# Performance work log

Hardware: AMD Instinct MI355X
Metric: run time of the kernel (lower is better)

Reference implementation:

```python
import jax, jax.numpy as jnp
import numpy as np

B, S, DM = 4, 2048, 512
H, D = 8, 64          # att_head, head_dim = att_dim // att_head
LEFT, RIGHT = 128, 128  # band_part(left_mask, right_mask)
LARGE = 1e30          # masked_softmax large number for fp32


def setup_inputs() -> dict:
    key = jax.random.key(0)
    ks = jax.random.split(key, 11)
    scale = 1.0 / np.sqrt(DM)
    x = jax.random.normal(ks[0], (B, S, DM), jnp.float32)
    Wq = jax.random.normal(ks[1], (DM, DM), jnp.float32) * scale
    bq = jnp.zeros((DM,), jnp.float32)
    Wk = jax.random.normal(ks[2], (DM, DM), jnp.float32) * scale
    bk = jnp.zeros((DM,), jnp.float32)
    Wv = jax.random.normal(ks[3], (DM, DM), jnp.float32) * scale
    bv = jnp.zeros((DM,), jnp.float32)
    Wo = jax.random.normal(ks[4], (DM, DM), jnp.float32) * scale
    bo = jnp.zeros((DM,), jnp.float32)
    x_len = jax.random.randint(ks[5], (B,), 0, 2048)
    return {"x": x, "Wq": Wq, "bq": bq, "Wk": Wk, "bk": bk,
            "Wv": Wv, "bv": bv, "Wo": Wo, "bo": bo, "x_len": x_len}


def reference(x, Wq, bq, Wk, bk, Wv, bv, Wo, bo, x_len):
    b, s, _ = x.shape
    # QKV projections, split into heads: [B,S,H,D]
    q = (x @ Wq + bq).reshape(b, s, H, D)
    k = (x @ Wk + bk).reshape(b, s, H, D)
    v = (x @ Wv + bv).reshape(b, s, H, D)
    # content energy: [B,H,Q,K], scaled by sqrt(head_dim)
    energy = jnp.einsum('bind,bjnd->bnij', q, k) / jnp.sqrt(jnp.float32(D))
    # banded mask (tf.linalg.band_part semantics): keep -LEFT <= j-i <= RIGHT
    i = jnp.arange(s)[:, None]
    j = jnp.arange(s)[None, :]
    band = ((j - i) <= RIGHT) & ((i - j) <= LEFT)            # [S,S]
    # key-length mask (tf.sequence_mask, expanded to [B,1,1,S])
    seq = jnp.arange(s)[None, :] < x_len[:, None]            # [B,S]
    mask = (band[None, None, :, :] & seq[:, None, None, :]).astype(energy.dtype)
    # masked softmax: energy - (1 - mask) * LARGE, softmax over keys
    att = jax.nn.softmax(energy - (1.0 - mask) * LARGE, axis=-1)
    # context: [B,Q,H,D] -> [B,S,H*D]
    ctx = jnp.einsum('bnij,bjnd->bind', att, v).reshape(b, s, H * D)
    # output projection (use_proj=True)
    return ctx @ Wo + bo
```

## Files before the change

### kernel.cpp

```cpp
#include <hip/hip_runtime.h>

#define S_LEN 2048
#define BATCH 4
#define DMODEL 512
#define NHEAD 8
#define HDIM 64
#define ROWS (BATCH * S_LEN)

using short8 = __attribute__((ext_vector_type(8))) short;
using f32x4  = __attribute__((ext_vector_type(4))) float;

__device__ __forceinline__ unsigned short f2bf(float f) {
  unsigned int u = __builtin_bit_cast(unsigned int, f);
  u += 0x7fffu + ((u >> 16) & 1u);
  return (unsigned short)(u >> 16);
}
__device__ __forceinline__ float bf2f(unsigned short h) {
  unsigned int u = ((unsigned int)h) << 16;
  return __builtin_bit_cast(float, u);
}
__device__ __forceinline__ void glds16(const void* g, void* l) {
  __builtin_amdgcn_global_load_lds((const __attribute__((address_space(1))) unsigned*)g,
                                   (__attribute__((address_space(3))) unsigned*)l, 16, 0, 0);
}

__global__ __launch_bounds__(256) void prep_kernel(const float* __restrict__ x,
                                                   const float* __restrict__ Wq,
                                                   const float* __restrict__ Wk,
                                                   const float* __restrict__ Wv,
                                                   const float* __restrict__ Wo,
                                                   unsigned short* __restrict__ xb,
                                                   unsigned short* __restrict__ WqkT,
                                                   unsigned short* __restrict__ WvT,
                                                   unsigned short* __restrict__ WoT,
                                                   float* __restrict__ xpart) {
  __shared__ float t[32][33];
  const int blk = blockIdx.x, tid = threadIdx.x;
  if (blk < 2048) {
    const int base = (blk * 256 + tid) * 8;
    float4 f0 = *(const float4*)(x + base);
    float4 f1 = *(const float4*)(x + base + 4);
    uint4 o;
    o.x = (unsigned)f2bf(f0.x) | ((unsigned)f2bf(f0.y) << 16);
    o.y = (unsigned)f2bf(f0.z) | ((unsigned)f2bf(f0.w) << 16);
    o.z = (unsigned)f2bf(f1.x) | ((unsigned)f2bf(f1.y) << 16);
    o.w = (unsigned)f2bf(f1.z) | ((unsigned)f2bf(f1.w) << 16);
    *(uint4*)(xb + base) = o;
    return;
  }
  if (blk < 3072) {
    const int tb = blk - 2048;
    const int which = tb >> 8, tile = tb & 255;
    const float* W = which == 0 ? Wq : which == 1 ? Wk : which == 2 ? Wv : Wo;
    unsigned short* WT = which == 0 ? WqkT : which == 1 ? (WqkT + 512 * 512)
                        : which == 2 ? WvT : WoT;
    const int tx = tid & 31, ty = tid >> 5;
    const int x0 = (tile & 15) * 32, y0 = (tile >> 4) * 32;
#pragma unroll
    for (int r = 0; r < 4; r++)
      t[ty + 8 * r][tx] = W[(size_t)(y0 + ty + 8 * r) * DMODEL + x0 + tx];
    __syncthreads();
#pragma unroll
    for (int r = 0; r < 4; r++)
      WT[(size_t)(x0 + ty + 8 * r) * DMODEL + y0 + tx] = f2bf(t[tx][ty + 8 * r]);
    return;
  }
  const int u = blk - 3072;
  const int b = u >> 4, cg = (u >> 3) & 1, rc = u & 7;
  const float* base = x + (size_t)(b * S_LEN + rc * 256) * DMODEL + cg * 256 + tid;
  float s = 0.f;
  for (int j = 0; j < 256; j++) s += base[(size_t)j * DMODEL];
  xpart[u * 256 + tid] = s;
}

__global__ __launch_bounds__(256, 2) void qkv_kernel(const unsigned short* __restrict__ xb,
                                                     const unsigned short* __restrict__ WqkT,
                                                     const unsigned short* __restrict__ WvT,
                                                     const float* __restrict__ bq,
                                                     const float* __restrict__ bk,
                                                     const float* __restrict__ bv,
                                                     const int* __restrict__ x_len,
                                                     const float* __restrict__ xpart,
                                                     unsigned short* __restrict__ Qb,
                                                     unsigned short* __restrict__ Kb,
                                                     unsigned short* __restrict__ Vt,
                                                     float* __restrict__ vsum) {
  __shared__ __align__(16) char smem[16384];
  const int bid = blockIdx.x;
  const int tid = threadIdx.x;
  if (bid >= 768) {
    const int u = bid - 768;
    const int b = u >> 5;
    const int wave = tid >> 6, lane = tid & 63;
    const int cg = lane >> 5, ko = (lane & 31) * 8;
    float xs[8] = {};
#pragma unroll
    for (int rc = 0; rc < 8; rc++) {
      const float* p = xpart + ((b * 16 + cg * 8 + rc) << 8) + ko;
      float4 a0 = *(const float4*)p;
      float4 a1 = *(const float4*)(p + 4);
      xs[0] += a0.x; xs[1] += a0.y; xs[2] += a0.z; xs[3] += a0.w;
      xs[4] += a1.x; xs[5] += a1.y; xs[6] += a1.z; xs[7] += a1.w;
    }
#pragma unroll
    for (int ci = 0; ci < 4; ci++) {
      const int f = (u & 31) * 16 + wave * 4 + ci;
      const uint4 wv = *(const uint4*)(WvT + (size_t)f * DMODEL + lane * 8);
      const unsigned int w[4] = {wv.x, wv.y, wv.z, wv.w};
      float acc = 0.f;
#pragma unroll
      for (int e = 0; e < 4; e++) {
        acc += xs[2 * e] * bf2f((unsigned short)(w[e] & 0xffffu));
        acc += xs[2 * e + 1] * bf2f((unsigned short)(w[e] >> 16));
      }
#pragma unroll
      for (int off = 1; off < 64; off <<= 1) acc += __shfl_xor(acc, off, 64);
      if (lane == 0) vsum[b * DMODEL + f] = acc + 2048.f * bv[f];
    }
    return;
  }
  const bool vmode = bid < 256;
  const unsigned short *A, *Bt;
  int m0, n0;
  if (vmode) {
    m0 = (bid & 3) * 128;
    n0 = (bid >> 2) * 128;
    A = WvT; Bt = xb;
  } else {
    const int q = bid - 256;
    m0 = (q >> 3) * 128;
    n0 = (q & 7) * 128;
    A = xb; Bt = WqkT;
    const int xl = x_len[m0 >> 11];
    const int s0 = m0 & 2047;
    if (n0 >= DMODEL) { if (s0 >= xl) return; }
    else if (s0 >= xl + 128) return;
  }
  char* As = smem;
  char* Bs = smem + 8192;
  const int wave = tid >> 6, lane = tid & 63;
  const int wr = wave >> 1, wc = wave & 1;
  const int lm = lane & 15, lq = lane >> 4;
  const int lr = lane >> 2;
  const int lc = (lane & 3) ^ ((lane >> 3) & 3);
  const unsigned short* gA0 = A + (size_t)(m0 + wave * 16 + lr) * DMODEL + lc * 8;
  const unsigned short* gA1 = A + (size_t)(m0 + (wave + 4) * 16 + lr) * DMODEL + lc * 8;
  const unsigned short* gB0 = Bt + (size_t)(n0 + wave * 16 + lr) * DMODEL + lc * 8;
  const unsigned short* gB1 = Bt + (size_t)(n0 + (wave + 4) * 16 + lr) * DMODEL + lc * 8;
  char* lA0 = As + wave * 1024 + lane * 16;
  char* lA1 = As + (wave + 4) * 1024 + lane * 16;
  char* lB0 = Bs + wave * 1024 + lane * 16;
  char* lB1 = Bs + (wave + 4) * 1024 + lane * 16;
  const int sw = (lm >> 1) & 3;
  int aoff[4], boff[4];
#pragma unroll
  for (int mi = 0; mi < 4; mi++) aoff[mi] = (wr * 64 + mi * 16 + lm) * 64 + (lq ^ sw) * 16;
#pragma unroll
  for (int ni = 0; ni < 4; ni++) boff[ni] = (wc * 64 + ni * 16 + lm) * 64 + (lq ^ sw) * 16;
  f32x4 acc[4][4] = {};
  for (int k0 = 0; k0 < DMODEL; k0 += 32) {
    __syncthreads();
    glds16(gA0 + k0, lA0);
    glds16(gA1 + k0, lA1);
    glds16(gB0 + k0, lB0);
    glds16(gB1 + k0, lB1);
    __syncthreads();
    short8 af[4], bfr[4];
#pragma unroll
    for (int mi = 0; mi < 4; mi++) af[mi] = *(const short8*)(As + aoff[mi]);
#pragma unroll
    for (int ni = 0; ni < 4; ni++) bfr[ni] = *(const short8*)(Bs + boff[ni]);
#pragma unroll
    for (int mi = 0; mi < 4; mi++)
#pragma unroll
      for (int ni = 0; ni < 4; ni++)
        acc[mi][ni] = __builtin_amdgcn_mfma_f32_16x16x32_bf16(af[mi], bfr[ni], acc[mi][ni], 0, 0, 0);
  }
#pragma unroll
  for (int mi = 0; mi < 4; mi++) {
    const int row0 = m0 + wr * 64 + mi * 16 + lq * 4;
#pragma unroll
    for (int ni = 0; ni < 4; ni++) {
      const int col = n0 + wc * 64 + ni * 16 + lm;
#pragma unroll
      for (int r = 0; r < 4; r++) {
        const int row = row0 + r;
        const float v = acc[mi][ni][r];
        if (vmode) {
          Vt[(size_t)row * ROWS + col] = f2bf(v + bv[row]);
        } else if (col < DMODEL) {
          Qb[(size_t)row * DMODEL + col] = f2bf(v + bq[col]);
        } else {
          Kb[(size_t)row * DMODEL + (col - DMODEL)] = f2bf(v + bk[col - DMODEL]);
        }
      }
    }
  }
}

__global__ __launch_bounds__(256) void attn_kernel(const unsigned short* __restrict__ Q,
                                                   const unsigned short* __restrict__ K,
                                                   const unsigned short* __restrict__ Vt,
                                                   const int* __restrict__ x_len,
                                                   const float* __restrict__ vsum,
                                                   const unsigned short* __restrict__ WoT,
                                                   const float* __restrict__ bo,
                                                   float* __restrict__ trow,
                                                   unsigned short* __restrict__ ctx) {
  __shared__ unsigned short Ks[32][72];
  __shared__ unsigned short Vs[64][40];
  __shared__ unsigned short Ps[4][16][40];
  const int tid = threadIdx.x;
  const int unit = blockIdx.x;
  const int wave = tid >> 6, lane = tid & 63;
  if (unit >= 1024) {
    const int u = unit - 1024;
    const int b = u >> 4;
    const float* vs = vsum + b * DMODEL + lane * 8;
    float vreg[8];
    *(float4*)vreg = *(const float4*)vs;
    *(float4*)(vreg + 4) = *(const float4*)(vs + 4);
#pragma unroll
    for (int ci = 0; ci < 8; ci++) {
      const int c = (u & 15) * 32 + wave * 8 + ci;
      const uint4 wv = *(const uint4*)(WoT + (size_t)c * DMODEL + lane * 8);
      const unsigned int w[4] = {wv.x, wv.y, wv.z, wv.w};
      float acc = 0.f;
#pragma unroll
      for (int e = 0; e < 4; e++) {
        acc += vreg[2 * e] * bf2f((unsigned short)(w[e] & 0xffffu));
        acc += vreg[2 * e + 1] * bf2f((unsigned short)(w[e] >> 16));
      }
#pragma unroll
      for (int off = 1; off < 64; off <<= 1) acc += __shfl_xor(acc, off, 64);
      if (lane == 0) trow[b * DMODEL + c] = bo[c] + acc * (1.f / 2048.f);
    }
    return;
  }
  const int b = unit >> 8, h = (unit >> 5) & 7;
  const int i0 = (unit & 31) * 64;
  const int xlen = x_len[b];
  const int t0 = min(S_LEN, xlen + 128);
  if ((i0 & ~127) >= t0) return;
  const int lm = lane & 15, lq = lane >> 4;
  const int q0 = i0 + wave * 16;
  const size_t qoff = (size_t)(b * S_LEN + q0 + lm) * DMODEL + h * HDIM + lq * 8;
  const short8 aq0 = *(const short8*)(Q + qoff);
  const short8 aq1 = *(const short8*)(Q + qoff + 32);
  const int krow = tid >> 3, kchk = (tid & 7) * 8;
  const int vdim = tid >> 2, vchk = (tid & 3) * 8;
  f32x4 oacc[4] = {};
  float lrow[4] = {0.f, 0.f, 0.f, 0.f};
  for (int kt = 0; kt < 10; kt++) {
    const int jt0 = i0 - 128 + kt * 32;
    if (jt0 + 31 < 0 || jt0 >= xlen) continue;
    __syncthreads();
    {
      const int jr = jt0 + krow;
      const int jrc = min(max(jr, 0), S_LEN - 1);
      *(uint4*)&Ks[krow][kchk] =
          *(const uint4*)(K + (size_t)(b * S_LEN + jrc) * DMODEL + h * HDIM + kchk);
      const int jv = jt0 + vchk;
      const int jvc = min(max(jv, 0), S_LEN - 8);
      *(uint4*)&Vs[vdim][vchk] =
          *(const uint4*)(Vt + (size_t)(h * HDIM + vdim) * ROWS + b * S_LEN + jvc);
    }
    __syncthreads();
    if (jt0 + 31 < q0 - 128 || jt0 > q0 + 143) continue;
    f32x4 sv[2];
#pragma unroll
    for (int sub = 0; sub < 2; sub++) {
      const short8 bk0 = *(const short8*)&Ks[sub * 16 + lm][lq * 8];
      const short8 bk1 = *(const short8*)&Ks[sub * 16 + lm][32 + lq * 8];
      f32x4 s = {};
      s = __builtin_amdgcn_mfma_f32_16x16x32_bf16(aq0, bk0, s, 0, 0, 0);
      s = __builtin_amdgcn_mfma_f32_16x16x32_bf16(aq1, bk1, s, 0, 0, 0);
      sv[sub] = s;
    }
    float p[2][4];
#pragma unroll
    for (int sub = 0; sub < 2; sub++) {
      const int j = jt0 + sub * 16 + lm;
      const bool jv = (j >= 0) && (j < xlen);
#pragma unroll
      for (int r = 0; r < 4; r++) {
        const int i = q0 + lq * 4 + r;
        const bool ok = jv && (j - i <= 128) && (i - j <= 128);
        const float pv = ok ? __expf(sv[sub][r] * 0.125f) : 0.f;
        p[sub][r] = pv;
        lrow[r] += pv;
      }
    }
#pragma unroll
    for (int r = 0; r < 4; r++) {
      Ps[wave][lq * 4 + r][lm] = f2bf(p[0][r]);
      Ps[wave][lq * 4 + r][16 + lm] = f2bf(p[1][r]);
    }
    const short8 pf = *(const short8*)&Ps[wave][lm][lq * 8];
#pragma unroll
    for (int dt = 0; dt < 4; dt++) {
      const short8 bv = *(const short8*)&Vs[dt * 16 + lm][lq * 8];
      oacc[dt] = __builtin_amdgcn_mfma_f32_16x16x32_bf16(pf, bv, oacc[dt], 0, 0, 0);
    }
  }
#pragma unroll
  for (int r = 0; r < 4; r++)
#pragma unroll
    for (int off = 1; off < 16; off <<= 1) lrow[r] += __shfl_xor(lrow[r], off, 64);
#pragma unroll
  for (int r = 0; r < 4; r++) {
    const int i = q0 + lq * 4 + r;
    const size_t obase = (size_t)(b * S_LEN + i) * DMODEL + h * HDIM;
    if (lrow[r] > 0.f) {
      const float inv = 1.f / lrow[r];
#pragma unroll
      for (int dt = 0; dt < 4; dt++)
        ctx[obase + dt * 16 + lm] = f2bf(oacc[dt][r] * inv);
    } else {
#pragma unroll
      for (int dt = 0; dt < 4; dt++)
        ctx[obase + dt * 16 + lm] =
            f2bf(vsum[(size_t)b * DMODEL + h * HDIM + dt * 16 + lm] * (1.f / 2048.f));
    }
  }
}

__global__ __launch_bounds__(256, 2) void out_kernel(const unsigned short* __restrict__ A,
                                                     const unsigned short* __restrict__ Bt,
                                                     const float* __restrict__ bias,
                                                     const int* __restrict__ x_len,
                                                     const float* __restrict__ trow,
                                                     float* __restrict__ out) {
  __shared__ __align__(16) char smem[16384];
  const int tid = threadIdx.x;
  const int m0 = (blockIdx.x >> 2) * 128, n0 = (blockIdx.x & 3) * 128;
  const int xl = x_len[m0 >> 11];
  if ((m0 & 2047) >= min(S_LEN, xl + 128)) {
    const float4 val = *(const float4*)(trow + (m0 >> 11) * DMODEL + n0 + (tid & 31) * 4);
    float* obase = out + (size_t)m0 * DMODEL + n0 + (tid & 31) * 4;
#pragma unroll
    for (int r = tid >> 5; r < 128; r += 8)
      *(float4*)(obase + (size_t)r * DMODEL) = val;
    return;
  }
  char* As = smem;
  char* Bs = smem + 8192;
  const int wave = tid >> 6, lane = tid & 63;
  const int wr = wave >> 1, wc = wave & 1;
  const int lm = lane & 15, lq = lane >> 4;
  const int lr = lane >> 2;
  const int lc = (lane & 3) ^ ((lane >> 3) & 3);
  const unsigned short* gA0 = A + (size_t)(m0 + wave * 16 + lr) * DMODEL + lc * 8;
  const unsigned short* gA1 = A + (size_t)(m0 + (wave + 4) * 16 + lr) * DMODEL + lc * 8;
  const unsigned short* gB0 = Bt + (size_t)(n0 + wave * 16 + lr) * DMODEL + lc * 8;
  const unsigned short* gB1 = Bt + (size_t)(n0 + (wave + 4) * 16 + lr) * DMODEL + lc * 8;
  char* lA0 = As + wave * 1024 + lane * 16;
  char* lA1 = As + (wave + 4) * 1024 + lane * 16;
  char* lB0 = Bs + wave * 1024 + lane * 16;
  char* lB1 = Bs + (wave + 4) * 1024 + lane * 16;
  const int sw = (lm >> 1) & 3;
  int aoff[4], boff[4];
#pragma unroll
  for (int mi = 0; mi < 4; mi++) aoff[mi] = (wr * 64 + mi * 16 + lm) * 64 + (lq ^ sw) * 16;
#pragma unroll
  for (int ni = 0; ni < 4; ni++) boff[ni] = (wc * 64 + ni * 16 + lm) * 64 + (lq ^ sw) * 16;
  f32x4 acc[4][4] = {};
  for (int k0 = 0; k0 < DMODEL; k0 += 32) {
    __syncthreads();
    glds16(gA0 + k0, lA0);
    glds16(gA1 + k0, lA1);
    glds16(gB0 + k0, lB0);
    glds16(gB1 + k0, lB1);
    __syncthreads();
    short8 af[4], bfr[4];
#pragma unroll
    for (int mi = 0; mi < 4; mi++) af[mi] = *(const short8*)(As + aoff[mi]);
#pragma unroll
    for (int ni = 0; ni < 4; ni++) bfr[ni] = *(const short8*)(Bs + boff[ni]);
#pragma unroll
    for (int mi = 0; mi < 4; mi++)
#pragma unroll
      for (int ni = 0; ni < 4; ni++)
        acc[mi][ni] = __builtin_amdgcn_mfma_f32_16x16x32_bf16(af[mi], bfr[ni], acc[mi][ni], 0, 0, 0);
  }
#pragma unroll
  for (int mi = 0; mi < 4; mi++) {
    const int row0 = m0 + wr * 64 + mi * 16 + lq * 4;
#pragma unroll
    for (int ni = 0; ni < 4; ni++) {
      const int col = n0 + wc * 64 + ni * 16 + lm;
#pragma unroll
      for (int r = 0; r < 4; r++)
        out[(size_t)(row0 + r) * DMODEL + col] = acc[mi][ni][r] + bias[col];
    }
  }
}

extern "C" void kernel_launch(void* const* d_in, const int* in_sizes, int n_in,
                              void* d_out, int out_size, void* d_ws, size_t ws_size,
                              hipStream_t stream) {
  (void)in_sizes; (void)n_in; (void)out_size; (void)ws_size;
  const float* x  = (const float*)d_in[0];
  const float* Wq = (const float*)d_in[1];
  const float* bq = (const float*)d_in[2];
  const float* Wk = (const float*)d_in[3];
  const float* bk = (const float*)d_in[4];
  const float* Wv = (const float*)d_in[5];
  const float* bv = (const float*)d_in[6];
  const float* Wo = (const float*)d_in[7];
  const float* bo = (const float*)d_in[8];
  const int* x_len = (const int*)d_in[9];

  char* ws = (char*)d_ws;
  const size_t MB = 1024 * 1024;
  unsigned short* xb   = (unsigned short*)(ws + 0 * MB);
  unsigned short* Qb   = (unsigned short*)(ws + 8 * MB);
  unsigned short* Kb   = (unsigned short*)(ws + 16 * MB);
  unsigned short* Vt   = (unsigned short*)(ws + 24 * MB);
  unsigned short* Cx   = (unsigned short*)(ws + 32 * MB);
  unsigned short* WqkT = (unsigned short*)(ws + 40 * MB);
  unsigned short* WvT  = (unsigned short*)(ws + 41 * MB);
  unsigned short* WoT  = (unsigned short*)(ws + 41 * MB + 512 * 1024);
  float* vsum          = (float*)(ws + 42 * MB);
  float* trow          = (float*)(ws + 42 * MB + 8192);
  float* xpart         = (float*)(ws + 43 * MB);

  prep_kernel<<<3136, 256, 0, stream>>>(x, Wq, Wk, Wv, Wo, xb, WqkT, WvT, WoT, xpart);
  qkv_kernel<<<896, 256, 0, stream>>>(xb, WqkT, WvT, bq, bk, bv, x_len, xpart,
                                      Qb, Kb, Vt, vsum);
  attn_kernel<<<1088, 256, 0, stream>>>(Qb, Kb, Vt, x_len, vsum, WoT, bo, trow, Cx);
  out_kernel<<<256, 256, 0, stream>>>(Cx, WoT, bo, x_len, trow, (float*)d_out);
}
```

Measured before the change: 150.1 us.

## Double K-step per barrier in GEMMs, widen attention key tiles, skip dead V tiles

The QKV and output GEMMs now stage 64-wide K slices per barrier pair instead of 32, with an 8-way XOR swizzle. This halves the number of synchronizations and gives each load more work. The attention kernel processes 64-key tiles instead of 32, halving its loop iterations and barriers at the cost of more LDS. V-projection blocks whose sequence tile lies entirely beyond x_len now exit early, but their Vt entries are left unwritten. That is only safe if every consumer masks those keys, which the attention path appears to do.

After: 147.3 us. Within noise of the previous version (-1.9%).

```diff
diff --git a/kernel.cpp b/kernel.cpp
--- a/kernel.cpp
+++ b/kernel.cpp
@@ -85,13 +85,13 @@
                                                      unsigned short* __restrict__ Kb,
                                                      unsigned short* __restrict__ Vt,
                                                      float* __restrict__ vsum) {
-  __shared__ __align__(16) char smem[16384];
+  __shared__ __align__(16) char smem[32768];
   const int bid = blockIdx.x;
   const int tid = threadIdx.x;
+  const int wave = tid >> 6, lane = tid & 63;
   if (bid >= 768) {
     const int u = bid - 768;
     const int b = u >> 5;
-    const int wave = tid >> 6, lane = tid & 63;
     const int cg = lane >> 5, ko = (lane & 31) * 8;
     float xs[8] = {};
 #pragma unroll
@@ -126,6 +126,7 @@
     m0 = (bid & 3) * 128;
     n0 = (bid >> 2) * 128;
     A = WvT; Bt = xb;
+    if ((n0 & 2047) >= x_len[n0 >> 11]) return;
   } else {
     const int q = bid - 256;
     m0 = (q >> 3) * 128;
@@ -137,44 +138,52 @@
     else if (s0 >= xl + 128) return;
   }
   char* As = smem;
-  char* Bs = smem + 8192;
-  const int wave = tid >> 6, lane = tid & 63;
+  char* Bs = smem + 16384;
   const int wr = wave >> 1, wc = wave & 1;
   const int lm = lane & 15, lq = lane >> 4;
-  const int lr = lane >> 2;
-  const int lc = (lane & 3) ^ ((lane >> 3) & 3);
-  const unsigned short* gA0 = A + (size_t)(m0 + wave * 16 + lr) * DMODEL + lc * 8;
-  const unsigned short* gA1 = A + (size_t)(m0 + (wave + 4) * 16 + lr) * DMODEL + lc * 8;
-  const unsigned short* gB0 = Bt + (size_t)(n0 + wave * 16 + lr) * DMODEL + lc * 8;
-  const unsigned short* gB1 = Bt + (size_t)(n0 + (wave + 4) * 16 + lr) * DMODEL + lc * 8;
-  char* lA0 = As + wave * 1024 + lane * 16;
-  char* lA1 = As + (wave + 4) * 1024 + lane * 16;
-  char* lB0 = Bs + wave * 1024 + lane * 16;
-  char* lB1 = Bs + (wave + 4) * 1024 + lane * 16;
-  const int sw = (lm >> 1) & 3;
-  int aoff[4], boff[4];
-#pragma unroll
-  for (int mi = 0; mi < 4; mi++) aoff[mi] = (wr * 64 + mi * 16 + lm) * 64 + (lq ^ sw) * 16;
-#pragma unroll
-  for (int ni = 0; ni < 4; ni++) boff[ni] = (wc * 64 + ni * 16 + lm) * 64 + (lq ^ sw) * 16;
+  const int srow = lane >> 3;
+  const int slc = (lane & 7) ^ (srow & 7);
+  const unsigned short* gA[4];
+  const unsigned short* gB[4];
+  char *lA[4], *lB[4];
+#pragma unroll
+  for (int i = 0; i < 4; i++) {
+    const int g = wave * 4 + i;
+    gA[i] = A + (size_t)(m0 + g * 8 + srow) * DMODEL + slc * 8;
+    gB[i] = Bt + (size_t)(n0 + g * 8 + srow) * DMODEL + slc * 8;
+    lA[i] = As + g * 1024 + lane * 16;
+    lB[i] = Bs + g * 1024 + lane * 16;
+  }
+  int aoff[4][2], boff[4][2];
+#pragma unroll
+  for (int mi = 0; mi < 4; mi++)
+#pragma unroll
+    for (int h = 0; h < 2; h++) {
+      aoff[mi][h] = (wr * 64 + mi * 16 + lm) * 128 + ((((h << 2) | lq)) ^ (lm & 7)) * 16;
+      boff[mi][h] = (wc * 64 + mi * 16 + lm) * 128 + ((((h << 2) | lq)) ^ (lm & 7)) * 16;
+    }
   f32x4 acc[4][4] = {};
-  for (int k0 = 0; k0 < DMODEL; k0 += 32) {
-    __syncthreads();
-    glds16(gA0 + k0, lA0);
-    glds16(gA1 + k0, lA1);
-    glds16(gB0 + k0, lB0);
-    glds16(gB1 + k0, lB1);
-    __syncthreads();
-    short8 af[4], bfr[4];
-#pragma unroll
-    for (int mi = 0; mi < 4; mi++) af[mi] = *(const short8*)(As + aoff[mi]);
-#pragma unroll
-    for (int ni = 0; ni < 4; ni++) bfr[ni] = *(const short8*)(Bs + boff[ni]);
-#pragma unroll
-    for (int mi = 0; mi < 4; mi++)
-#pragma unroll
-      for (int ni = 0; ni < 4; ni++)
-        acc[mi][ni] = __builtin_amdgcn_mfma_f32_16x16x32_bf16(af[mi], bfr[ni], acc[mi][ni], 0, 0, 0);
+  for (int k0 = 0; k0 < DMODEL; k0 += 64) {
+    __syncthreads();
+#pragma unroll
+    for (int i = 0; i < 4; i++) {
+      glds16(gA[i] + k0, lA[i]);
+      glds16(gB[i] + k0, lB[i]);
+    }
+    __syncthreads();
+#pragma unroll
+    for (int h = 0; h < 2; h++) {
+      short8 af[4], bfr[4];
+#pragma unroll
+      for (int mi = 0; mi < 4; mi++) af[mi] = *(const short8*)(As + aoff[mi][h]);
+#pragma unroll
+      for (int ni = 0; ni < 4; ni++) bfr[ni] = *(const short8*)(Bs + boff[ni][h]);
+#pragma unroll
+      for (int mi = 0; mi < 4; mi++)
+#pragma unroll
+        for (int ni = 0; ni < 4; ni++)
+          acc[mi][ni] = __builtin_amdgcn_mfma_f32_16x16x32_bf16(af[mi], bfr[ni], acc[mi][ni], 0, 0, 0);
+    }
   }
 #pragma unroll
   for (int mi = 0; mi < 4; mi++) {
@@ -207,9 +216,9 @@
                                                    const float* __restrict__ bo,
                                                    float* __restrict__ trow,
                                                    unsigned short* __restrict__ ctx) {
-  __shared__ unsigned short Ks[32][72];
-  __shared__ unsigned short Vs[64][40];
-  __shared__ unsigned short Ps[4][16][40];
+  __shared__ unsigned short Ks[64][72];
+  __shared__ unsigned short Vs[64][72];
+  __shared__ unsigned short Ps[4][16][72];
   const int tid = threadIdx.x;
   const int unit = blockIdx.x;
   const int wave = tid >> 6, lane = tid & 63;
@@ -247,29 +256,32 @@
   const size_t qoff = (size_t)(b * S_LEN + q0 + lm) * DMODEL + h * HDIM + lq * 8;
   const short8 aq0 = *(const short8*)(Q + qoff);
   const short8 aq1 = *(const short8*)(Q + qoff + 32);
-  const int krow = tid >> 3, kchk = (tid & 7) * 8;
-  const int vdim = tid >> 2, vchk = (tid & 3) * 8;
+  const int sr = tid >> 3, sc = (tid & 7) * 8;
   f32x4 oacc[4] = {};
   float lrow[4] = {0.f, 0.f, 0.f, 0.f};
-  for (int kt = 0; kt < 10; kt++) {
-    const int jt0 = i0 - 128 + kt * 32;
-    if (jt0 + 31 < 0 || jt0 >= xlen) continue;
+  for (int kt = 0; kt < 5; kt++) {
+    const int jt0 = i0 - 128 + kt * 64;
+    if (jt0 + 63 < 0 || jt0 >= xlen) continue;
     __syncthreads();
     {
-      const int jr = jt0 + krow;
-      const int jrc = min(max(jr, 0), S_LEN - 1);
-      *(uint4*)&Ks[krow][kchk] =
-          *(const uint4*)(K + (size_t)(b * S_LEN + jrc) * DMODEL + h * HDIM + kchk);
-      const int jv = jt0 + vchk;
-      const int jvc = min(max(jv, 0), S_LEN - 8);
-      *(uint4*)&Vs[vdim][vchk] =
-          *(const uint4*)(Vt + (size_t)(h * HDIM + vdim) * ROWS + b * S_LEN + jvc);
-    }
-    __syncthreads();
-    if (jt0 + 31 < q0 - 128 || jt0 > q0 + 143) continue;
-    f32x4 sv[2];
-#pragma unroll
-    for (int sub = 0; sub < 2; sub++) {
+      const int jr0 = min(max(jt0 + sr, 0), S_LEN - 1);
+      const int jr1 = min(max(jt0 + sr + 32, 0), S_LEN - 1);
+      *(uint4*)&Ks[sr][sc] =
+          *(const uint4*)(K + (size_t)(b * S_LEN + jr0) * DMODEL + h * HDIM + sc);
+      *(uint4*)&Ks[sr + 32][sc] =
+          *(const uint4*)(K + (size_t)(b * S_LEN + jr1) * DMODEL + h * HDIM + sc);
+      const int jvc = min(max(jt0 + sc, 0), S_LEN - 8);
+      *(uint4*)&Vs[sr][sc] =
+          *(const uint4*)(Vt + (size_t)(h * HDIM + sr) * ROWS + b * S_LEN + jvc);
+      *(uint4*)&Vs[sr + 32][sc] =
+          *(const uint4*)(Vt + (size_t)(h * HDIM + sr + 32) * ROWS + b * S_LEN + jvc);
+    }
+    __syncthreads();
+    if (jt0 + 63 < q0 - 128 || jt0 > q0 + 143) continue;
+
+    f32x4 sv[4];
+#pragma unroll
+    for (int sub = 0; sub < 4; sub++) {
       const short8 bk0 = *(const short8*)&Ks[sub * 16 + lm][lq * 8];
       const short8 bk1 = *(const short8*)&Ks[sub * 16 + lm][32 + lq * 8];
       f32x4 s = {};
@@ -277,9 +289,9 @@
       s = __builtin_amdgcn_mfma_f32_16x16x32_bf16(aq1, bk1, s, 0, 0, 0);
       sv[sub] = s;
     }
-    float p[2][4];
-#pragma unroll
-    for (int sub = 0; sub < 2; sub++) {
+    float p[4][4];
+#pragma unroll
+    for (int sub = 0; sub < 4; sub++) {
       const int j = jt0 + sub * 16 + lm;
       const bool jv = (j >= 0) && (j < xlen);
 #pragma unroll
@@ -292,15 +304,18 @@
       }
     }
 #pragma unroll
-    for (int r = 0; r < 4; r++) {
-      Ps[wave][lq * 4 + r][lm] = f2bf(p[0][r]);
-      Ps[wave][lq * 4 + r][16 + lm] = f2bf(p[1][r]);
-    }
-    const short8 pf = *(const short8*)&Ps[wave][lm][lq * 8];
+    for (int sub = 0; sub < 4; sub++)
+#pragma unroll
+      for (int r = 0; r < 4; r++)
+        Ps[wave][lq * 4 + r][sub * 16 + lm] = f2bf(p[sub][r]);
+    const short8 pf0 = *(const short8*)&Ps[wave][lm][lq * 8];
+    const short8 pf1 = *(const short8*)&Ps[wave][lm][32 + lq * 8];
 #pragma unroll
     for (int dt = 0; dt < 4; dt++) {
-      const short8 bv = *(const short8*)&Vs[dt * 16 + lm][lq * 8];
-      oacc[dt] = __builtin_amdgcn_mfma_f32_16x16x32_bf16(pf, bv, oacc[dt], 0, 0, 0);
+      const short8 bv0 = *(const short8*)&Vs[dt * 16 + lm][lq * 8];
+      const short8 bv1 = *(const short8*)&Vs[dt * 16 + lm][32 + lq * 8];
+      oacc[dt] = __builtin_amdgcn_mfma_f32_16x16x32_bf16(pf0, bv0, oacc[dt], 0, 0, 0);
+      oacc[dt] = __builtin_amdgcn_mfma_f32_16x16x32_bf16(pf1, bv1, oacc[dt], 0, 0, 0);
     }
   }
 #pragma unroll
@@ -331,7 +346,7 @@
                                                      const int* __restrict__ x_len,
                                                      const float* __restrict__ trow,
                                                      float* __restrict__ out) {
-  __shared__ __align__(16) char smem[16384];
+  __shared__ __align__(16) char smem[32768];
   const int tid = threadIdx.x;
   const int m0 = (blockIdx.x >> 2) * 128, n0 = (blockIdx.x & 3) * 128;
   const int xl = x_len[m0 >> 11];
@@ -344,44 +359,53 @@
     return;
   }
   char* As = smem;
-  char* Bs = smem + 8192;
+  char* Bs = smem + 16384;
   const int wave = tid >> 6, lane = tid & 63;
   const int wr = wave >> 1, wc = wave & 1;
   const int lm = lane & 15, lq = lane >> 4;
-  const int lr = lane >> 2;
-  const int lc = (lane & 3) ^ ((lane >> 3) & 3);
-  const unsigned short* gA0 = A + (size_t)(m0 + wave * 16 + lr) * DMODEL + lc * 8;
-  const unsigned short* gA1 = A + (size_t)(m0 + (wave + 4) * 16 + lr) * DMODEL + lc * 8;
-  const unsigned short* gB0 = Bt + (size_t)(n0 + wave * 16 + lr) * DMODEL + lc * 8;
-  const unsigned short* gB1 = Bt + (size_t)(n0 + (wave + 4) * 16 + lr) * DMODEL + lc * 8;
-  char* lA0 = As + wave * 1024 + lane * 16;
-  char* lA1 = As + (wave + 4) * 1024 + lane * 16;
-  char* lB0 = Bs + wave * 1024 + lane * 16;
-  char* lB1 = Bs + (wave + 4) * 1024 + lane * 16;
-  const int sw = (lm >> 1) & 3;
-  int aoff[4], boff[4];
-#pragma unroll
-  for (int mi = 0; mi < 4; mi++) aoff[mi] = (wr * 64 + mi * 16 + lm) * 64 + (lq ^ sw) * 16;
-#pragma unroll
-  for (int ni = 0; ni < 4; ni++) boff[ni] = (wc * 64 + ni * 16 + lm) * 64 + (lq ^ sw) * 16;
+  const int srow = lane >> 3;
+  const int slc = (lane & 7) ^ (srow & 7);
+  const unsigned short* gA[4];
+  const unsigned short* gB[4];
+  char *lA[4], *lB[4];
+#pragma unroll
+  for (int i = 0; i < 4; i++) {
+    const int g = wave * 4 + i;
+    gA[i] = A + (size_t)(m0 + g * 8 + srow) * DMODEL + slc * 8;
+    gB[i] = Bt + (size_t)(n0 + g * 8 + srow) * DMODEL + slc * 8;
+    lA[i] = As + g * 1024 + lane * 16;
+    lB[i] = Bs + g * 1024 + lane * 16;
+  }
+  int aoff[4][2], boff[4][2];
+#pragma unroll
+  for (int mi = 0; mi < 4; mi++)
+#pragma unroll
+    for (int h = 0; h < 2; h++) {
+      aoff[mi][h] = (wr * 64 + mi * 16 + lm) * 128 + ((((h << 2) | lq)) ^ (lm & 7)) * 16;
+      boff[mi][h] = (wc * 64 + mi * 16 + lm) * 128 + ((((h << 2) | lq)) ^ (lm & 7)) * 16;
+    }
   f32x4 acc[4][4] = {};
-  for (int k0 = 0; k0 < DMODEL; k0 += 32) {
-    __syncthreads();
-    glds16(gA0 + k0, lA0);
-    glds16(gA1 + k0, lA1);
-    glds16(gB0 + k0, lB0);
-    glds16(gB1 + k0, lB1);
-    __syncthreads();
-    short8 af[4], bfr[4];
-#pragma unroll
-    for (int mi = 0; mi < 4; mi++) af[mi] = *(const short8*)(As + aoff[mi]);
-#pragma unroll
-    for (int ni = 0; ni < 4; ni++) bfr[ni] = *(const short8*)(Bs + boff[ni]);
-#pragma unroll
-    for (int mi = 0; mi < 4; mi++)
-#pragma unroll
-      for (int ni = 0; ni < 4; ni++)
-        acc[mi][ni] = __builtin_amdgcn_mfma_f32_16x16x32_bf16(af[mi], bfr[ni], acc[mi][ni], 0, 0, 0);
+  for (int k0 = 0; k0 < DMODEL; k0 += 64) {
+    __syncthreads();
+#pragma unroll
+    for (int i = 0; i < 4; i++) {
+      glds16(gA[i] + k0, lA[i]);
+      glds16(gB[i] + k0, lB[i]);
+    }
+    __syncthreads();
+#pragma unroll
+    for (int h = 0; h < 2; h++) {
+      short8 af[4], bfr[4];
+#pragma unroll
+      for (int mi = 0; mi < 4; mi++) af[mi] = *(const short8*)(As + aoff[mi][h]);
+#pragma unroll
+      for (int ni = 0; ni < 4; ni++) bfr[ni] = *(const short8*)(Bs + boff[ni][h]);
+#pragma unroll
+      for (int mi = 0; mi < 4; mi++)
+#pragma unroll
+        for (int ni = 0; ni < 4; ni++)
+          acc[mi][ni] = __builtin_amdgcn_mfma_f32_16x16x32_bf16(af[mi], bfr[ni], acc[mi][ni], 0, 0, 0);
+    }
   }
 #pragma unroll
   for (int mi = 0; mi < 4; mi++) {
```
